# Kernel optimization log

Hardware: AMD Instinct MI355X
Metric: run time of the kernel (lower is better)

The kernel has to match this reference:

```python
import jax, jax.numpy as jnp
import numpy as np

CONF_THRESHOLD = 0.5
NO_CONF_PENALTY = 10.0
BIG = 1e30  # stands in for 'exclude non-confident pixels from the min'


def setup_inputs() -> dict:
    key = jax.random.key(0)
    k1, k2, k3, k4 = jax.random.split(key, 4)
    B, H, W, N = 8, 256, 256, 100
    return {
        "loc_pred": jax.random.normal(k1, (B, H, W, 2), jnp.float32),
        "uncertainty": jax.random.normal(k2, (B, H, W, 1), jnp.float32),
        "true_locations": jax.random.uniform(k3, (B, N, 2), jnp.float32),
        "prob_map": jax.random.uniform(k4, (B, 1, H, W), jnp.float32),
    }


def _per_batch(loc, unc, true_locs, prob):
    # loc: [H,W,2], unc: [H,W,1], true_locs: [N,2], prob: [1,H,W]
    H, W, _ = loc.shape
    P = H * W
    a = loc.reshape(P, 2)                 # candidate predicted locations (row-major, as torch.nonzero order)
    u = unc[..., 0].reshape(P)
    conf = prob.reshape(P) > CONF_THRESHOLD
    valid = (true_locs[:, 0] >= 0) & (true_locs[:, 1] >= 0)  # [N]

    # cdist p=2 via |a|^2 + |b|^2 - 2 a.b (avoids [P,N,2] intermediate)
    a2 = jnp.sum(a * a, axis=1)           # [P]
    b2 = jnp.sum(true_locs * true_locs, axis=1)  # [N]
    d2 = a2[:, None] + b2[None, :] - 2.0 * (a @ true_locs.T)  # [P,N]
    d = jnp.sqrt(jnp.maximum(d2, 0.0))

    # min over confident pixels, per true location (torch: dist_matrix.min(dim=0))
    min_d = jnp.where(conf[:, None], d, BIG).min(axis=0)  # [N]

    # torch quirk: weighted by exp(-uncertainty) of the FIRST k confident pixels
    # (row-major order), k = number of valid true locations.
    rank = jnp.cumsum(valid) - 1                                 # position of each valid true loc among valid ones
    perm = jnp.argsort(jnp.logical_not(conf), stable=True)      # confident pixels first, original order preserved
    uw_sorted = jnp.exp(-u[perm])                                # [P], first num_conf entries are confident pixels
    w = uw_sorted[jnp.clip(rank, 0, P - 1)]                      # [N]

    weighted = jnp.where(valid, min_d * w, 0.0)
    nv = valid.sum()
    nc = conf.sum()
    loc_loss = weighted.sum() / jnp.maximum(nv, 1).astype(weighted.dtype)
    # original: skip batch if no valid true locs; add 10.0 if no confident pixel
    return jnp.where(nv == 0, 0.0, jnp.where(nc == 0, NO_CONF_PENALTY, loc_loss))


def reference(loc_pred, uncertainty, true_locations, prob_map):
    B = loc_pred.shape[0]
    per_batch = jax.vmap(_per_batch)(loc_pred, uncertainty, true_locations, prob_map)  # [B]
    return per_batch.sum() / B
```

## Files before the change

### kernel.cpp

```cpp
#include <hip/hip_runtime.h>

#define NLOC 100
#define TPB 512
#define NWAVE 8
#define NLW 13
#define CHUNK 1024
#define STEP 256


__global__ __launch_bounds__(TPB, 2)
void k_all(const float* __restrict__ loc, const float* __restrict__ unc,
           const float* __restrict__ prob, const float* __restrict__ tloc,
           unsigned* __restrict__ pm, unsigned* __restrict__ wts,
           unsigned* __restrict__ nc, unsigned* __restrict__ valbuf,
           float* __restrict__ out, int P, int B, int nsub)
{
    __shared__ float2 s_t[NLW * NWAVE];
    __shared__ float s_d[NLOC];

    const int tid  = (int)threadIdx.x;
    const int wv   = tid >> 6;
    const int lane = tid & 63;
    const int sub  = (int)blockIdx.x;
    const int b    = (int)blockIdx.y;

    for (int i = tid; i < NLW * NWAVE; i += TPB)
        s_t[i] = (i < NLOC) ? reinterpret_cast<const float2*>(tloc)[b * NLOC + i]
                            : make_float2(-1.f, -1.f);
    __syncthreads();

    float nbx[NLW], nby[NLW], m[NLW];
    #pragma unroll
    for (int i = 0; i < NLW; ++i) {
        float2 t = s_t[wv + i * NWAVE];
        nbx[i] = -2.0f * t.x;
        nby[i] = -2.0f * t.y;
        m[i] = 3.0e38f;
    }

    const float* locf  = loc  + (size_t)b * P * 2;
    const float* probp = prob + (size_t)b * P;
    const int base = sub * CHUNK;

    #pragma unroll
    for (int s = 0; s < CHUNK / STEP; ++s) {
        const int p0 = base + s * STEP + lane * 4;
        float4 pr = *reinterpret_cast<const float4*>(probp + p0);
        float4 lA = *reinterpret_cast<const float4*>(locf + 2 * p0);
        float4 lB = *reinterpret_cast<const float4*>(locf + 2 * p0 + 4);
        float x0 = (pr.x > 0.5f) ? lA.x : 1.0e15f, y0 = (pr.x > 0.5f) ? lA.y : 1.0e15f;
        float x1 = (pr.y > 0.5f) ? lA.z : 1.0e15f, y1 = (pr.y > 0.5f) ? lA.w : 1.0e15f;
        float x2 = (pr.z > 0.5f) ? lB.x : 1.0e15f, y2 = (pr.z > 0.5f) ? lB.y : 1.0e15f;
        float x3 = (pr.w > 0.5f) ? lB.z : 1.0e15f, y3 = (pr.w > 0.5f) ? lB.w : 1.0e15f;
        float a0 = __builtin_fmaf(x0, x0, y0 * y0);
        float a1 = __builtin_fmaf(x1, x1, y1 * y1);
        float a2 = __builtin_fmaf(x2, x2, y2 * y2);
        float a3 = __builtin_fmaf(x3, x3, y3 * y3);
        #pragma unroll
        for (int i = 0; i < NLW; ++i) {
            float d0 = __builtin_fmaf(y0, nby[i], __builtin_fmaf(x0, nbx[i], a0));
            float d1 = __builtin_fmaf(y1, nby[i], __builtin_fmaf(x1, nbx[i], a1));
            float d2 = __builtin_fmaf(y2, nby[i], __builtin_fmaf(x2, nbx[i], a2));
            float d3 = __builtin_fmaf(y3, nby[i], __builtin_fmaf(x3, nbx[i], a3));
            m[i] = fminf(m[i], fminf(fminf(d0, d1), fminf(d2, d3)));
        }
    }

    #pragma unroll
    for (int i = 0; i < NLW; ++i) {
        float mm = m[i];
        #pragma unroll
        for (int off = 32; off; off >>= 1)
            mm = fminf(mm, __shfl_xor(mm, off));
        int n = wv + i * NWAVE;
        if (lane == 0 && n < NLOC) {
            float b2 = 0.25f * __builtin_fmaf(nbx[i], nbx[i], nby[i] * nby[i]);
            unsigned v = __float_as_uint(fmaxf(mm + b2, 0.0f)) & 0x7FFFFFFFu;
            __hip_atomic_store(&pm[((size_t)b * NLOC + n) * nsub + sub], v,
                               __ATOMIC_RELAXED, __HIP_MEMORY_SCOPE_AGENT);
        }
    }

    if (sub != 0) return;


    if (wv == 0) {
        const float* up = unc + (size_t)b * P;
        const int nchunks = (P + 63) >> 6;
        int nconf = 0;
        for (int c = 0; c < nchunks; ++c) {
            if (nconf >= NLOC) break;
            int p = (c << 6) + lane;
            bool inb = p < P;
            float pv = probp[inb ? p : 0];
            bool conf = inb && (pv > 0.5f);
            unsigned long long mask = __ballot(conf);
            int pref = __popcll(mask & ((1ull << lane) - 1ull));
            int r = nconf + pref;
            if (conf && r < NLOC)
                __hip_atomic_store(&wts[b * NLOC + r], __float_as_uint(expf(-up[p])),
                                   __ATOMIC_RELAXED, __HIP_MEMORY_SCOPE_AGENT);
            nconf += __popcll(mask);
        }
        if (nconf < NLOC) {
            int nnon = 0;
            for (int c = 0; c < nchunks; ++c) {
                if (nconf + nnon >= NLOC) break;
                int p = (c << 6) + lane;
                bool inb = p < P;
                float pv = probp[inb ? p : 0];
                bool nonc = inb && !(pv > 0.5f);
                unsigned long long mask = __ballot(nonc);
                int pref = __popcll(mask & ((1ull << lane) - 1ull));
                int r = nconf + nnon + pref;
                if (nonc && r < NLOC)
                    __hip_atomic_store(&wts[b * NLOC + r], __float_as_uint(expf(-up[p])),
                                       __ATOMIC_RELAXED, __HIP_MEMORY_SCOPE_AGENT);
                nnon += __popcll(mask);
            }
        }
        if (lane == 0)
            __hip_atomic_store(&nc[b], (nconf > 0) ? 1u : 0u,
                               __ATOMIC_RELAXED, __HIP_MEMORY_SCOPE_AGENT);
    }

    for (int j = wv; j < NLOC; j += NWAVE) {
        const unsigned* slots = pm + ((size_t)b * NLOC + j) * nsub;
        float mv = 3.0e38f;
        for (int s0 = lane; s0 < nsub; s0 += 64) {
            unsigned u = __hip_atomic_load(&slots[s0], __ATOMIC_RELAXED,
                                           __HIP_MEMORY_SCOPE_AGENT);
            while (u & 0x80000000u)
                u = __hip_atomic_load(&slots[s0], __ATOMIC_RELAXED,
                                      __HIP_MEMORY_SCOPE_AGENT);
            mv = fminf(mv, __uint_as_float(u));
        }
        #pragma unroll
        for (int off = 32; off; off >>= 1)
            mv = fminf(mv, __shfl_xor(mv, off));
        if (lane == 0) s_d[j] = sqrtf(mv);
    }
    __syncthreads();
    if (wv != 0) return;

    float sum = 0.0f;
    int vbase = 0;
    for (int c = 0; c < (NLOC + 63) / 64; ++c) {
        int j = c * 64 + lane;
        bool valid = false;
        if (j < NLOC) {
            float2 t = s_t[j];
            valid = (t.x >= 0.f) && (t.y >= 0.f);
        }
        unsigned long long mask = __ballot(valid);
        int rank = vbase + __popcll(mask & ((1ull << lane) - 1ull));
        if (valid) {
            unsigned wu = __hip_atomic_load(&wts[b * NLOC + rank],
                                            __ATOMIC_RELAXED, __HIP_MEMORY_SCOPE_AGENT);
            while (wu & 0x80000000u)
                wu = __hip_atomic_load(&wts[b * NLOC + rank],
                                       __ATOMIC_RELAXED, __HIP_MEMORY_SCOPE_AGENT);
            sum += s_d[j] * __uint_as_float(wu);
        }
        vbase += __popcll(mask);
    }
    #pragma unroll
    for (int off = 32; off; off >>= 1)
        sum += __shfl_xor(sum, off);

    if (lane == 0) {
        unsigned ncv = __hip_atomic_load(&nc[b], __ATOMIC_RELAXED,
                                         __HIP_MEMORY_SCOPE_AGENT);
        while (ncv & 0x80000000u)
            ncv = __hip_atomic_load(&nc[b], __ATOMIC_RELAXED,
                                    __HIP_MEMORY_SCOPE_AGENT);
        float val = (vbase == 0) ? 0.0f
                    : ((ncv == 0u) ? 10.0f : sum / (float)vbase);
        __hip_atomic_store(&valbuf[b], __float_as_uint(val) & 0x7FFFFFFFu,
                           __ATOMIC_RELAXED, __HIP_MEMORY_SCOPE_AGENT);
    }

    if (b == 0) {
        float v = 0.0f;
        if (lane < B) {
            unsigned u = __hip_atomic_load(&valbuf[lane], __ATOMIC_RELAXED,
                                           __HIP_MEMORY_SCOPE_AGENT);
            while (u & 0x80000000u)
                u = __hip_atomic_load(&valbuf[lane], __ATOMIC_RELAXED,
                                      __HIP_MEMORY_SCOPE_AGENT);
            v = __uint_as_float(u);
        }
        #pragma unroll
        for (int off = 32; off; off >>= 1)
            v += __shfl_xor(v, off);
        if (lane == 0) out[0] = v / (float)B;
    }
}

extern "C" void kernel_launch(void* const* d_in, const int* in_sizes, int n_in,
                              void* d_out, int out_size, void* d_ws, size_t ws_size,
                              hipStream_t stream)
{
    const float* loc  = (const float*)d_in[0];
    const float* unc  = (const float*)d_in[1];
    const float* tloc = (const float*)d_in[2];
    const float* prob = (const float*)d_in[3];
    float* out = (float*)d_out;

    int B = in_sizes[2] / (2 * NLOC);
    int P = in_sizes[1] / B;
    int nsub = (P + CHUNK - 1) / CHUNK;

    unsigned* pm   = (unsigned*)d_ws;
    unsigned* wts  = pm + (size_t)B * NLOC * nsub;
    unsigned* ncp  = wts + (size_t)B * NLOC;
    unsigned* valb = ncp + B;

    hipLaunchKernelGGL(k_all, dim3(nsub, B), dim3(TPB), 0, stream,
                       loc, unc, prob, tloc, pm, wts, ncp, valb,
                       out, P, B, nsub);
}
```

Measured before the change: 24.60 us.

## Move per-batch finalize into a dedicated extra block with batched slot polling

Adds one extra block per batch that does the weight selection and partial-min reduction while the compute blocks only produce partial minima. Wave 0 builds the first-k weights in shared memory and waves 1-7 poll the partial slots, issuing all loads first and then spinning, so the reduction overlaps with the weight scan. Weights and the confidence flag no longer go through global memory. The cost is one extra block per batch, plus a reliance on nsub being at most 64 so each lane holds one slot.

```diff
diff --git a/kernel.cpp b/kernel.cpp
--- a/kernel.cpp
+++ b/kernel.cpp
@@ -6,17 +6,16 @@
 #define NLW 13
 #define CHUNK 1024
 #define STEP 256
+#define NPW 15
 
 
 __global__ __launch_bounds__(TPB, 2)
 void k_all(const float* __restrict__ loc, const float* __restrict__ unc,
            const float* __restrict__ prob, const float* __restrict__ tloc,
-           unsigned* __restrict__ pm, unsigned* __restrict__ wts,
-           unsigned* __restrict__ nc, unsigned* __restrict__ valbuf,
+           unsigned* __restrict__ pm, unsigned* __restrict__ valbuf,
            float* __restrict__ out, int P, int B, int nsub)
 {
     __shared__ float2 s_t[NLW * NWAVE];
-    __shared__ float s_d[NLOC];
 
     const int tid  = (int)threadIdx.x;
     const int wv   = tid >> 6;
@@ -24,65 +23,69 @@
     const int sub  = (int)blockIdx.x;
     const int b    = (int)blockIdx.y;
 
+    const float* locf  = loc  + (size_t)b * P * 2;
+    const float* probp = prob + (size_t)b * P;
+
     for (int i = tid; i < NLW * NWAVE; i += TPB)
         s_t[i] = (i < NLOC) ? reinterpret_cast<const float2*>(tloc)[b * NLOC + i]
                             : make_float2(-1.f, -1.f);
     __syncthreads();
 
-    float nbx[NLW], nby[NLW], m[NLW];
-    #pragma unroll
-    for (int i = 0; i < NLW; ++i) {
-        float2 t = s_t[wv + i * NWAVE];
-        nbx[i] = -2.0f * t.x;
-        nby[i] = -2.0f * t.y;
-        m[i] = 3.0e38f;
-    }
-
-    const float* locf  = loc  + (size_t)b * P * 2;
-    const float* probp = prob + (size_t)b * P;
-    const int base = sub * CHUNK;
-
-    #pragma unroll
-    for (int s = 0; s < CHUNK / STEP; ++s) {
-        const int p0 = base + s * STEP + lane * 4;
-        float4 pr = *reinterpret_cast<const float4*>(probp + p0);
-        float4 lA = *reinterpret_cast<const float4*>(locf + 2 * p0);
-        float4 lB = *reinterpret_cast<const float4*>(locf + 2 * p0 + 4);
-        float x0 = (pr.x > 0.5f) ? lA.x : 1.0e15f, y0 = (pr.x > 0.5f) ? lA.y : 1.0e15f;
-        float x1 = (pr.y > 0.5f) ? lA.z : 1.0e15f, y1 = (pr.y > 0.5f) ? lA.w : 1.0e15f;
-        float x2 = (pr.z > 0.5f) ? lB.x : 1.0e15f, y2 = (pr.z > 0.5f) ? lB.y : 1.0e15f;
-        float x3 = (pr.w > 0.5f) ? lB.z : 1.0e15f, y3 = (pr.w > 0.5f) ? lB.w : 1.0e15f;
-        float a0 = __builtin_fmaf(x0, x0, y0 * y0);
-        float a1 = __builtin_fmaf(x1, x1, y1 * y1);
-        float a2 = __builtin_fmaf(x2, x2, y2 * y2);
-        float a3 = __builtin_fmaf(x3, x3, y3 * y3);
+    if (sub < nsub) {
+        float nbx[NLW], nby[NLW], m[NLW];
         #pragma unroll
         for (int i = 0; i < NLW; ++i) {
-            float d0 = __builtin_fmaf(y0, nby[i], __builtin_fmaf(x0, nbx[i], a0));
-            float d1 = __builtin_fmaf(y1, nby[i], __builtin_fmaf(x1, nbx[i], a1));
-            float d2 = __builtin_fmaf(y2, nby[i], __builtin_fmaf(x2, nbx[i], a2));
-            float d3 = __builtin_fmaf(y3, nby[i], __builtin_fmaf(x3, nbx[i], a3));
-            m[i] = fminf(m[i], fminf(fminf(d0, d1), fminf(d2, d3)));
-        }
-    }
-
-    #pragma unroll
-    for (int i = 0; i < NLW; ++i) {
-        float mm = m[i];
-        #pragma unroll
-        for (int off = 32; off; off >>= 1)
-            mm = fminf(mm, __shfl_xor(mm, off));
-        int n = wv + i * NWAVE;
-        if (lane == 0 && n < NLOC) {
-            float b2 = 0.25f * __builtin_fmaf(nbx[i], nbx[i], nby[i] * nby[i]);
-            unsigned v = __float_as_uint(fmaxf(mm + b2, 0.0f)) & 0x7FFFFFFFu;
-            __hip_atomic_store(&pm[((size_t)b * NLOC + n) * nsub + sub], v,
-                               __ATOMIC_RELAXED, __HIP_MEMORY_SCOPE_AGENT);
-        }
-    }
-
-    if (sub != 0) return;
-
+            float2 t = s_t[wv + i * NWAVE];
+            nbx[i] = -2.0f * t.x;
+            nby[i] = -2.0f * t.y;
+            m[i] = 3.0e38f;
+        }
+
+        const int base = sub * CHUNK;
+        #pragma unroll
+        for (int s = 0; s < CHUNK / STEP; ++s) {
+            const int p0 = base + s * STEP + lane * 4;
+            float4 pr = *reinterpret_cast<const float4*>(probp + p0);
+            float4 lA = *reinterpret_cast<const float4*>(locf + 2 * p0);
+            float4 lB = *reinterpret_cast<const float4*>(locf + 2 * p0 + 4);
+            float x0 = (pr.x > 0.5f) ? lA.x : 1.0e15f, y0 = (pr.x > 0.5f) ? lA.y : 1.0e15f;
+            float x1 = (pr.y > 0.5f) ? lA.z : 1.0e15f, y1 = (pr.y > 0.5f) ? lA.w : 1.0e15f;
+            float x2 = (pr.z > 0.5f) ? lB.x : 1.0e15f, y2 = (pr.z > 0.5f) ? lB.y : 1.0e15f;
+            float x3 = (pr.w > 0.5f) ? lB.z : 1.0e15f, y3 = (pr.w > 0.5f) ? lB.w : 1.0e15f;
+            float a0 = __builtin_fmaf(x0, x0, y0 * y0);
+            float a1 = __builtin_fmaf(x1, x1, y1 * y1);
+            float a2 = __builtin_fmaf(x2, x2, y2 * y2);
+            float a3 = __builtin_fmaf(x3, x3, y3 * y3);
+            #pragma unroll
+            for (int i = 0; i < NLW; ++i) {
+                float d0 = __builtin_fmaf(y0, nby[i], __builtin_fmaf(x0, nbx[i], a0));
+                float d1 = __builtin_fmaf(y1, nby[i], __builtin_fmaf(x1, nbx[i], a1));
+                float d2 = __builtin_fmaf(y2, nby[i], __builtin_fmaf(x2, nbx[i], a2));
+                float d3 = __builtin_fmaf(y3, nby[i], __builtin_fmaf(x3, nbx[i], a3));
+                m[i] = fminf(m[i], fminf(fminf(d0, d1), fminf(d2, d3)));
+            }
+        }
+
+        #pragma unroll
+        for (int i = 0; i < NLW; ++i) {
+            float mm = m[i];
+            #pragma unroll
+            for (int off = 32; off; off >>= 1)
+                mm = fminf(mm, __shfl_xor(mm, off));
+            int n = wv + i * NWAVE;
+            if (lane == 0 && n < NLOC) {
+                float b2 = 0.25f * __builtin_fmaf(nbx[i], nbx[i], nby[i] * nby[i]);
+                unsigned v = __float_as_uint(fmaxf(mm + b2, 0.0f)) & 0x7FFFFFFFu;
+                __hip_atomic_store(&pm[((size_t)b * NLOC + n) * nsub + sub], v,
+                                   __ATOMIC_RELAXED, __HIP_MEMORY_SCOPE_AGENT);
+            }
+        }
+        return;
+    }
+
+    __shared__ float s_d[NLOC];
+    __shared__ float s_w[NLOC];
+    __shared__ unsigned s_nc;
 
     if (wv == 0) {
         const float* up = unc + (size_t)b * P;
@@ -97,9 +100,7 @@
             unsigned long long mask = __ballot(conf);
             int pref = __popcll(mask & ((1ull << lane) - 1ull));
             int r = nconf + pref;
-            if (conf && r < NLOC)
-                __hip_atomic_store(&wts[b * NLOC + r], __float_as_uint(expf(-up[p])),
-                                   __ATOMIC_RELAXED, __HIP_MEMORY_SCOPE_AGENT);
+            if (conf && r < NLOC) s_w[r] = expf(-up[p]);
             nconf += __popcll(mask);
         }
         if (nconf < NLOC) {
@@ -113,32 +114,47 @@
                 unsigned long long mask = __ballot(nonc);
                 int pref = __popcll(mask & ((1ull << lane) - 1ull));
                 int r = nconf + nnon + pref;
-                if (nonc && r < NLOC)
-                    __hip_atomic_store(&wts[b * NLOC + r], __float_as_uint(expf(-up[p])),
-                                       __ATOMIC_RELAXED, __HIP_MEMORY_SCOPE_AGENT);
+                if (nonc && r < NLOC) s_w[r] = expf(-up[p]);
                 nnon += __popcll(mask);
             }
         }
-        if (lane == 0)
-            __hip_atomic_store(&nc[b], (nconf > 0) ? 1u : 0u,
-                               __ATOMIC_RELAXED, __HIP_MEMORY_SCOPE_AGENT);
-    }
-
-    for (int j = wv; j < NLOC; j += NWAVE) {
-        const unsigned* slots = pm + ((size_t)b * NLOC + j) * nsub;
-        float mv = 3.0e38f;
-        for (int s0 = lane; s0 < nsub; s0 += 64) {
-            unsigned u = __hip_atomic_load(&slots[s0], __ATOMIC_RELAXED,
-                                           __HIP_MEMORY_SCOPE_AGENT);
-            while (u & 0x80000000u)
-                u = __hip_atomic_load(&slots[s0], __ATOMIC_RELAXED,
-                                      __HIP_MEMORY_SCOPE_AGENT);
-            mv = fminf(mv, __uint_as_float(u));
-        }
-        #pragma unroll
-        for (int off = 32; off; off >>= 1)
-            mv = fminf(mv, __shfl_xor(mv, off));
-        if (lane == 0) s_d[j] = sqrtf(mv);
+        if (lane == 0) s_nc = (nconf > 0) ? 1u : 0u;
+    } else {
+        const int jb = wv - 1;
+        unsigned uu[NPW];
+        #pragma unroll
+        for (int t = 0; t < NPW; ++t) {
+            int j = jb + t * 7;
+            uu[t] = 0u;
+            if (j < NLOC && lane < nsub)
+                uu[t] = __hip_atomic_load(&pm[((size_t)b * NLOC + j) * nsub + lane],
+                                          __ATOMIC_RELAXED, __HIP_MEMORY_SCOPE_AGENT);
+        }
+        #pragma unroll
+        for (int t = 0; t < NPW; ++t) {
+            int j = jb + t * 7;
+            if (j < NLOC && lane < nsub)
+                while (uu[t] & 0x80000000u)
+                    uu[t] = __hip_atomic_load(&pm[((size_t)b * NLOC + j) * nsub + lane],
+                                              __ATOMIC_RELAXED, __HIP_MEMORY_SCOPE_AGENT);
+        }
+        float uf[NPW];
+        #pragma unroll
+        for (int t = 0; t < NPW; ++t) {
+            int j = jb + t * 7;
+            uf[t] = (j < NLOC && lane < nsub) ? __uint_as_float(uu[t]) : 3.0e38f;
+        }
+        #pragma unroll
+        for (int off = 32; off; off >>= 1) {
+            #pragma unroll
+            for (int t = 0; t < NPW; ++t)
+                uf[t] = fminf(uf[t], __shfl_xor(uf[t], off));
+        }
+        #pragma unroll
+        for (int t = 0; t < NPW; ++t) {
+            int j = jb + t * 7;
+            if (j < NLOC && lane == 0) s_d[j] = sqrtf(uf[t]);
+        }
     }
     __syncthreads();
     if (wv != 0) return;
@@ -154,14 +170,7 @@
         }
         unsigned long long mask = __ballot(valid);
         int rank = vbase + __popcll(mask & ((1ull << lane) - 1ull));
-        if (valid) {
-            unsigned wu = __hip_atomic_load(&wts[b * NLOC + rank],
-                                            __ATOMIC_RELAXED, __HIP_MEMORY_SCOPE_AGENT);
-            while (wu & 0x80000000u)
-                wu = __hip_atomic_load(&wts[b * NLOC + rank],
-                                       __ATOMIC_RELAXED, __HIP_MEMORY_SCOPE_AGENT);
-            sum += s_d[j] * __uint_as_float(wu);
-        }
+        if (valid) sum += s_d[j] * s_w[rank];
         vbase += __popcll(mask);
     }
     #pragma unroll
@@ -169,13 +178,8 @@
         sum += __shfl_xor(sum, off);
 
     if (lane == 0) {
-        unsigned ncv = __hip_atomic_load(&nc[b], __ATOMIC_RELAXED,
-                                         __HIP_MEMORY_SCOPE_AGENT);
-        while (ncv & 0x80000000u)
-            ncv = __hip_atomic_load(&nc[b], __ATOMIC_RELAXED,
-                                    __HIP_MEMORY_SCOPE_AGENT);
         float val = (vbase == 0) ? 0.0f
-                    : ((ncv == 0u) ? 10.0f : sum / (float)vbase);
+                    : ((s_nc == 0u) ? 10.0f : sum / (float)vbase);
         __hip_atomic_store(&valbuf[b], __float_as_uint(val) & 0x7FFFFFFFu,
                            __ATOMIC_RELAXED, __HIP_MEMORY_SCOPE_AGENT);
     }
@@ -212,11 +216,8 @@
     int nsub = (P + CHUNK - 1) / CHUNK;
 
     unsigned* pm   = (unsigned*)d_ws;
-    unsigned* wts  = pm + (size_t)B * NLOC * nsub;
-    unsigned* ncp  = wts + (size_t)B * NLOC;
-    unsigned* valb = ncp + B;
-
-    hipLaunchKernelGGL(k_all, dim3(nsub, B), dim3(TPB), 0, stream,
-                       loc, unc, prob, tloc, pm, wts, ncp, valb,
-                       out, P, B, nsub);
+    unsigned* valb = pm + (size_t)B * NLOC * nsub;
+
+    hipLaunchKernelGGL(k_all, dim3(nsub + 1, B), dim3(TPB), 0, stream,
+                       loc, unc, prob, tloc, pm, valb, out, P, B, nsub);
 }
```

Result: slower. 26.15 us (+6.3%).
